# Kernel optimization log

Measured on AMD Instinct MI355X. Metric: run time of the kernel, lower is better.

Reference implementation:

```python
import jax, jax.numpy as jnp
import numpy as np

# Config (mirrors init_kwargs)
N_PARTS = 4
N_DATASETS = 4
N_VOLUMES = 12
N_TRANSFORMS = 1
TEMP = 0.1
EPS = 1e-6
BS = N_PARTS * N_DATASETS * N_VOLUMES          # 192
N = BS * (N_TRANSFORMS + 1)                    # 384 total rows
PD = N_PARTS * N_DATASETS                      # 16
C, H, W = 32, 48, 48


def setup_inputs() -> dict:
    key = jax.random.key(0)
    k1, k2 = jax.random.split(key)
    reg_pred = jax.random.normal(k1, (N, C, H, W), dtype=jnp.float32)
    mean_representations = jax.random.normal(k2, (N_DATASETS, C, H, W), dtype=jnp.float32)
    return {"reg_pred": reg_pred, "mean_representations": mean_representations}


def reference(reg_pred, mean_representations):
    X = reg_pred.reshape(N, -1)                                  # [N, D]
    ds_id = (jnp.arange(N) // N_PARTS) % N_DATASETS              # dataset id per row
    Mn = mean_representations.reshape(N_DATASETS, -1)[ds_id]     # [N, D] per-row mean
    Z = X - Mn                                                   # demeaned
    # cosine similarity with per-vector norm clamped at eps (torch CosineSimilarity)
    nrm = jnp.maximum(jnp.linalg.norm(Z, axis=1), EPS)
    Zn = Z / nrm[:, None]
    S = (Zn @ Zn.T) / TEMP                                       # [N, N] scaled cos sims
    E = jnp.exp(S)
    # negative (denominator) set for anchor a: all j with j % PD != a % PD
    rem = jnp.arange(N) % PD
    neg_mask = rem[:, None] != rem[None, :]
    Dsum = jnp.sum(E * neg_mask, axis=1)                         # [N]

    p = jnp.arange(BS)
    i1 = p
    i2 = BS + p
    i3 = (p + PD) % N
    i4 = (BS + p + PD) % N

    def pair_loss(a, b):
        # Faithful to original: BOTH terms use the (a,b) numerator similarity
        num = S[a, b]
        en = jnp.exp(num)
        return -(num - jnp.log(en + Dsum[a])) - (num - jnp.log(en + Dsum[b]))

    total = (pair_loss(i1, i2) + pair_loss(i3, i4)
             + pair_loss(i1, i3) + pair_loss(i2, i4)).sum()
    return total / (N_TRANSFORMS * 3 * BS)
```

## Files before the change

### kernel.cpp

```cpp
#include <hip/hip_runtime.h>
#include <hip/hip_bf16.h>
#include <stdint.h>

#define NR 384
#define DD 73728
#define PDV 16
#define BSV 192
#define KSPLIT 128
#define KCH 576
#define BK 32

typedef __bf16 bf16;
typedef __attribute__((ext_vector_type(8))) __bf16 bf16x8;
typedef __attribute__((ext_vector_type(4))) float f32x4;

__device__ __forceinline__ void async_copy16(const float* g, float* l) {
    __builtin_amdgcn_global_load_lds(
        (__attribute__((address_space(1))) void*)g,
        (__attribute__((address_space(3))) void*)l,
        16, 0, 0);
}

__global__ __launch_bounds__(256) void k_gram(const float* __restrict__ X,
                                              const float* __restrict__ M,
                                              float* __restrict__ Gp) {
    __shared__ float ashF[128 * BK];
    __shared__ float bshF[128 * BK];
    __shared__ float msh[4 * BK];
    const int tid  = threadIdx.x;
    const int lane = tid & 63;
    const int w    = tid >> 6;
    const int quad = lane >> 4;
    const int l15  = lane & 15;
    const int l7   = lane & 7;
    const int wm   = w & 1, wn = w >> 1;

    int bx   = blockIdx.x;
    int tile = bx % 6;
    int ks   = bx / 6;
    int tm = (tile < 3) ? 0 : ((tile < 5) ? 1 : 2);
    int tn = (tile < 3) ? tile : ((tile < 5) ? (tile - 2) : 2);
    int rowA0 = tm * 128, rowB0 = tn * 128;
    size_t k0 = (size_t)ks * KCH;

    f32x4 acc[4][4];
#pragma unroll
    for (int i = 0; i < 4; ++i)
#pragma unroll
        for (int j = 0; j < 4; ++j) acc[i][j] = (f32x4){0.f, 0.f, 0.f, 0.f};

    for (int kb = 0; kb < KCH; kb += BK) {
        size_t kbase = k0 + kb;
        __syncthreads();
#pragma unroll
        for (int t = 0; t < 4; ++t) {
            int S   = t * 256 + tid;
            int row = S >> 3;
            int sp  = S & 7;
            int gs  = sp ^ (row & 7);
            size_t gco = kbase + gs * 4;
            int base = (t * 256 + w * 64) * 4;
            async_copy16(X + (size_t)(rowA0 + row) * DD + gco, &ashF[base]);
            async_copy16(X + (size_t)(rowB0 + row) * DD + gco, &bshF[base]);
        }
        if (tid < 32) {
            float4 m4 = *(const float4*)(M + (size_t)(tid >> 3) * DD + kbase + (tid & 7) * 4);
            *(float4*)&msh[tid * 4] = m4;
        }
        __syncthreads();

        f32x4 mu = *(const f32x4*)&msh[(l15 >> 2) * BK + quad * 8];
        f32x4 mv = *(const f32x4*)&msh[(l15 >> 2) * BK + quad * 8 + 4];

        bf16x8 af[4], bfv[4];
#pragma unroll
        for (int i = 0; i < 4; ++i) {
            int r = wm * 64 + i * 16 + l15;
            f32x4 u = *(const f32x4*)&ashF[r * BK + (((quad << 1) ^ l7) << 2)];
            f32x4 v = *(const f32x4*)&ashF[r * BK + ((((quad << 1) | 1) ^ l7) << 2)];
            bf16x8 f;
            f[0] = (bf16)(u[0] - mu[0]); f[1] = (bf16)(u[1] - mu[1]);
            f[2] = (bf16)(u[2] - mu[2]); f[3] = (bf16)(u[3] - mu[3]);
            f[4] = (bf16)(v[0] - mv[0]); f[5] = (bf16)(v[1] - mv[1]);
            f[6] = (bf16)(v[2] - mv[2]); f[7] = (bf16)(v[3] - mv[3]);
            af[i] = f;
        }
#pragma unroll
        for (int j = 0; j < 4; ++j) {
            int r = wn * 64 + j * 16 + l15;
            f32x4 u = *(const f32x4*)&bshF[r * BK + (((quad << 1) ^ l7) << 2)];
            f32x4 v = *(const f32x4*)&bshF[r * BK + ((((quad << 1) | 1) ^ l7) << 2)];
            bf16x8 f;
            f[0] = (bf16)(u[0] - mu[0]); f[1] = (bf16)(u[1] - mu[1]);
            f[2] = (bf16)(u[2] - mu[2]); f[3] = (bf16)(u[3] - mu[3]);
            f[4] = (bf16)(v[0] - mv[0]); f[5] = (bf16)(v[1] - mv[1]);
            f[6] = (bf16)(v[2] - mv[2]); f[7] = (bf16)(v[3] - mv[3]);
            bfv[j] = f;
        }
#pragma unroll
        for (int i = 0; i < 4; ++i)
#pragma unroll
            for (int j = 0; j < 4; ++j)
                acc[i][j] = __builtin_amdgcn_mfma_f32_16x16x32_bf16(
                    af[i], bfv[j], acc[i][j], 0, 0, 0);
    }

    float* gp = Gp + ((size_t)(ks * 6 + tile) << 14);
#pragma unroll
    for (int i = 0; i < 4; ++i) {
        int lr0 = wm * 64 + i * 16 + quad * 4;
#pragma unroll
        for (int j = 0; j < 4; ++j) {
            int lc = wn * 64 + j * 16 + l15;
#pragma unroll
            for (int r = 0; r < 4; ++r)
                gp[(lr0 + r) * 128 + lc] = acc[i][j][r];
        }
    }
}

__global__ __launch_bounds__(256) void k_red(const float* __restrict__ Gp,
                                             float* __restrict__ G,
                                             float* __restrict__ invn,
                                             float* __restrict__ out) {
    int t    = blockIdx.x * 256 + threadIdx.x;
    if (t == 0) out[0] = 0.0f;
    int tile = t >> 14;
    int idx  = t & 16383;
    int lr   = idx >> 7, lc = idx & 127;
    const float* p = Gp + ((size_t)tile << 14) + idx;
    float s = 0.0f;
#pragma unroll 8
    for (int ks = 0; ks < KSPLIT; ++ks) s += p[(size_t)ks * 98304];
    int tm = (tile < 3) ? 0 : ((tile < 5) ? 1 : 2);
    int tn = (tile < 3) ? tile : ((tile < 5) ? (tile - 2) : 2);
    int a = tm * 128 + lr, b = tn * 128 + lc;
    G[(size_t)a * NR + b] = s;
    G[(size_t)b * NR + a] = s;
    if (a == b) invn[a] = 1.0f / fmaxf(sqrtf(s), 1e-6f);
}

__global__ __launch_bounds__(256) void k_dsum(const float* __restrict__ G,
                                              const float* __restrict__ invn,
                                              float* __restrict__ out) {
    const int lane = threadIdx.x & 63;
    const int a    = blockIdx.x * 4 + (threadIdx.x >> 6);
    float ia  = invn[a];
    int arem  = a & 15;
    float acc = 0.0f;
    for (int b = lane; b < NR; b += 64) {
        float s = G[(size_t)a * NR + b] * ia * invn[b] * 10.0f;
        if ((b & 15) != arem) acc += expf(s);
    }
#pragma unroll
    for (int o = 32; o > 0; o >>= 1) acc += __shfl_down(acc, o);
    if (lane == 0) {
        float Dsa = acc;
        int pr[4];
        if (a < 16)       { pr[0] = 192 + a; pr[1] = a + 16;  pr[2] = a + 192; pr[3] = a + 368; }
        else if (a < 192) { pr[0] = 192 + a; pr[1] = a + 16;  pr[2] = a + 192; pr[3] = a - 16; }
        else if (a < 368) { pr[0] = a - 192; pr[1] = a + 16;  pr[2] = a - 192; pr[3] = a - 16; }
        else              { pr[0] = a - 192; pr[1] = a - 368; pr[2] = a - 192; pr[3] = a - 16; }
        float t = 0.0f;
#pragma unroll
        for (int s = 0; s < 4; ++s) {
            int b = pr[s];
            float num = G[(size_t)a * NR + b] * ia * invn[b] * 10.0f;
            t += -num + logf(expf(num) + Dsa);
        }
        atomicAdd(out, t * (1.0f / 576.0f));
    }
}

extern "C" void kernel_launch(void* const* d_in, const int* in_sizes, int n_in,
                              void* d_out, int out_size, void* d_ws, size_t ws_size,
                              hipStream_t stream) {
    const float* X = (const float*)d_in[0];
    const float* M = (const float*)d_in[1];
    float* out = (float*)d_out;

    char* ws = (char*)d_ws;
    float* Gp   = (float*)ws;
    float* G    = Gp + (size_t)KSPLIT * 6 * 16384;
    float* invn = G + (size_t)NR * NR;

    k_gram<<<dim3(6 * KSPLIT), dim3(256), 0, stream>>>(X, M, Gp);
    k_red<<<dim3(384), dim3(256), 0, stream>>>(Gp, G, invn, out);
    k_dsum<<<dim3(NR / 4), dim3(256), 0, stream>>>(G, invn, out);
}
```

Measured before the change: 199.5 us.

## Stage demeaned bf16 tiles in LDS with wider K steps instead of async fp32 copies

Replaces the async global-to-LDS fp32 copies with register loads that subtract the mean and convert to bf16 before writing into padded LDS rows. The K step grows from 32 to 96, so each block does 6 iterations with three MFMA sub-steps each, cutting barrier count and halving LDS footprint per element. The per-fragment fp32-to-bf16 conversion is no longer repeated at MFMA-read time, and launch bounds request 3 blocks per CU. The trade-off is giving up the async copy path, so global loads now stall through registers, and the mean is loaded per element rather than once per tile.

```diff
diff --git a/kernel.cpp b/kernel.cpp
--- a/kernel.cpp
+++ b/kernel.cpp
@@ -8,31 +8,24 @@
 #define BSV 192
 #define KSPLIT 128
 #define KCH 576
-#define BK 32
+#define BK 96
+#define RS 104
 
 typedef __bf16 bf16;
+typedef __attribute__((ext_vector_type(4))) __bf16 bf16x4;
 typedef __attribute__((ext_vector_type(8))) __bf16 bf16x8;
 typedef __attribute__((ext_vector_type(4))) float f32x4;
 
-__device__ __forceinline__ void async_copy16(const float* g, float* l) {
-    __builtin_amdgcn_global_load_lds(
-        (__attribute__((address_space(1))) void*)g,
-        (__attribute__((address_space(3))) void*)l,
-        16, 0, 0);
-}
-
-__global__ __launch_bounds__(256) void k_gram(const float* __restrict__ X,
-                                              const float* __restrict__ M,
-                                              float* __restrict__ Gp) {
-    __shared__ float ashF[128 * BK];
-    __shared__ float bshF[128 * BK];
-    __shared__ float msh[4 * BK];
+__global__ __launch_bounds__(256, 3) void k_gram(const float* __restrict__ X,
+                                                 const float* __restrict__ M,
+                                                 float* __restrict__ Gp) {
+    __shared__ bf16 ash[128 * RS];
+    __shared__ bf16 bsh[128 * RS];
     const int tid  = threadIdx.x;
     const int lane = tid & 63;
     const int w    = tid >> 6;
     const int quad = lane >> 4;
     const int l15  = lane & 15;
-    const int l7   = lane & 7;
     const int wm   = w & 1, wn = w >> 1;
 
     int bx   = blockIdx.x;
@@ -40,7 +33,8 @@
     int ks   = bx / 6;
     int tm = (tile < 3) ? 0 : ((tile < 5) ? 1 : 2);
     int tn = (tile < 3) ? tile : ((tile < 5) ? (tile - 2) : 2);
-    int rowA0 = tm * 128, rowB0 = tn * 128;
+    const float* Xa = X + (size_t)(tm * 128) * DD;
+    const float* Xb = X + (size_t)(tn * 128) * DD;
     size_t k0 = (size_t)ks * KCH;
 
     f32x4 acc[4][4];
@@ -49,60 +43,48 @@
 #pragma unroll
         for (int j = 0; j < 4; ++j) acc[i][j] = (f32x4){0.f, 0.f, 0.f, 0.f};
 
-    for (int kb = 0; kb < KCH; kb += BK) {
-        size_t kbase = k0 + kb;
+    for (int it = 0; it < 6; ++it) {
+        size_t kbase = k0 + it * BK;
         __syncthreads();
 #pragma unroll
-        for (int t = 0; t < 4; ++t) {
-            int S   = t * 256 + tid;
-            int row = S >> 3;
-            int sp  = S & 7;
-            int gs  = sp ^ (row & 7);
-            size_t gco = kbase + gs * 4;
-            int base = (t * 256 + w * 64) * 4;
-            async_copy16(X + (size_t)(rowA0 + row) * DD + gco, &ashF[base]);
-            async_copy16(X + (size_t)(rowB0 + row) * DD + gco, &bshF[base]);
-        }
-        if (tid < 32) {
-            float4 m4 = *(const float4*)(M + (size_t)(tid >> 3) * DD + kbase + (tid & 7) * 4);
-            *(float4*)&msh[tid * 4] = m4;
+        for (int l = 0; l < 12; ++l) {
+            int idx  = l * 256 + tid;
+            int row  = idx / 24;
+            int kseg = idx - row * 24;
+            size_t gk = kbase + kseg * 4;
+            const float4 m4 = *(const float4*)(M + (size_t)((row >> 2) & 3) * DD + gk);
+            const float4 xa = *(const float4*)(Xa + (size_t)row * DD + gk);
+            const float4 xb = *(const float4*)(Xb + (size_t)row * DD + gk);
+            bf16x4 za, zb;
+            za[0] = (bf16)(xa.x - m4.x); za[1] = (bf16)(xa.y - m4.y);
+            za[2] = (bf16)(xa.z - m4.z); za[3] = (bf16)(xa.w - m4.w);
+            zb[0] = (bf16)(xb.x - m4.x); zb[1] = (bf16)(xb.y - m4.y);
+            zb[2] = (bf16)(xb.z - m4.z); zb[3] = (bf16)(xb.w - m4.w);
+            *(bf16x4*)&ash[row * RS + kseg * 4] = za;
+            *(bf16x4*)&bsh[row * RS + kseg * 4] = zb;
         }
         __syncthreads();
 
-        f32x4 mu = *(const f32x4*)&msh[(l15 >> 2) * BK + quad * 8];
-        f32x4 mv = *(const f32x4*)&msh[(l15 >> 2) * BK + quad * 8 + 4];
-
-        bf16x8 af[4], bfv[4];
 #pragma unroll
-        for (int i = 0; i < 4; ++i) {
-            int r = wm * 64 + i * 16 + l15;
-            f32x4 u = *(const f32x4*)&ashF[r * BK + (((quad << 1) ^ l7) << 2)];
-            f32x4 v = *(const f32x4*)&ashF[r * BK + ((((quad << 1) | 1) ^ l7) << 2)];
-            bf16x8 f;
-            f[0] = (bf16)(u[0] - mu[0]); f[1] = (bf16)(u[1] - mu[1]);
-            f[2] = (bf16)(u[2] - mu[2]); f[3] = (bf16)(u[3] - mu[3]);
-            f[4] = (bf16)(v[0] - mv[0]); f[5] = (bf16)(v[1] - mv[1]);
-            f[6] = (bf16)(v[2] - mv[2]); f[7] = (bf16)(v[3] - mv[3]);
-            af[i] = f;
+        for (int c = 0; c < 3; ++c) {
+            bf16x8 af[4], bfv[4];
+#pragma unroll
+            for (int i = 0; i < 4; ++i) {
+                int r = wm * 64 + i * 16 + l15;
+                af[i] = *(const bf16x8*)&ash[r * RS + c * 32 + quad * 8];
+            }
+#pragma unroll
+            for (int j = 0; j < 4; ++j) {
+                int r = wn * 64 + j * 16 + l15;
+                bfv[j] = *(const bf16x8*)&bsh[r * RS + c * 32 + quad * 8];
+            }
+#pragma unroll
+            for (int i = 0; i < 4; ++i)
+#pragma unroll
+                for (int j = 0; j < 4; ++j)
+                    acc[i][j] = __builtin_amdgcn_mfma_f32_16x16x32_bf16(
+                        af[i], bfv[j], acc[i][j], 0, 0, 0);
         }
-#pragma unroll
-        for (int j = 0; j < 4; ++j) {
-            int r = wn * 64 + j * 16 + l15;
-            f32x4 u = *(const f32x4*)&bshF[r * BK + (((quad << 1) ^ l7) << 2)];
-            f32x4 v = *(const f32x4*)&bshF[r * BK + ((((quad << 1) | 1) ^ l7) << 2)];
-            bf16x8 f;
-            f[0] = (bf16)(u[0] - mu[0]); f[1] = (bf16)(u[1] - mu[1]);
-            f[2] = (bf16)(u[2] - mu[2]); f[3] = (bf16)(u[3] - mu[3]);
-            f[4] = (bf16)(v[0] - mv[0]); f[5] = (bf16)(v[1] - mv[1]);
-            f[6] = (bf16)(v[2] - mv[2]); f[7] = (bf16)(v[3] - mv[3]);
-            bfv[j] = f;
-        }
-#pragma unroll
-        for (int i = 0; i < 4; ++i)
-#pragma unroll
-            for (int j = 0; j < 4; ++j)
-                acc[i][j] = __builtin_amdgcn_mfma_f32_16x16x32_bf16(
-                    af[i], bfv[j], acc[i][j], 0, 0, 0);
     }
 
     float* gp = Gp + ((size_t)(ks * 6 + tile) << 14);
```

After: 266.6 us. 1.34x slower.
